# Kernel optimization log

Measured on AMD Instinct MI355X. Metric: run time of the kernel, lower is better.

The kernel has to match this reference:

```python
import jax, jax.numpy as jnp
import numpy as np
import math

DIM = 1024
NUM_HEADS = 16
HEAD_DIM = 64
SEQ_LEN = 2048
ATTN_SCALE = 0.12


def cosine_norm(x, eps=1e-12):
    # unit-normalize along last dim
    return x * jax.lax.rsqrt(jnp.sum(x * x, axis=-1, keepdims=True) + eps)


def rotary_tables(T, head_dim):
    dim_quarter = max(1, head_dim // 4)
    angular_freq = (1.0 / 1024.0) ** jnp.linspace(0.0, 1.0, dim_quarter, dtype=jnp.float32)
    angular_freq = jnp.concatenate([angular_freq, jnp.zeros(dim_quarter, dtype=jnp.float32)])  # [head_dim//2]
    t = jnp.arange(T, dtype=jnp.float32)
    theta = t[:, None] * angular_freq[None, :]  # [T, head_dim//2]
    return jnp.cos(theta), jnp.sin(theta)


def apply_rotary(x_BTHD, cos, sin):
    # cos/sin: [T, head_dim//2] -> broadcast [1, T, 1, head_dim//2]
    c = cos[None, :, None, :]
    s = sin[None, :, None, :]
    x1, x2 = jnp.split(x_BTHD, 2, axis=-1)
    y1 = x1 * c + x2 * s
    y2 = -x1 * s + x2 * c
    return jnp.concatenate([y1, y2], axis=-1)


def setup_inputs() -> dict:
    key = jax.random.key(0)
    ks = jax.random.split(key, 6)
    x = jax.random.normal(ks[0], (1, SEQ_LEN, DIM), dtype=jnp.float32)
    init_std = 0.02
    Wq = jax.random.normal(ks[1], (DIM, NUM_HEADS * HEAD_DIM), dtype=jnp.float32) * init_std
    Wk = jax.random.normal(ks[2], (DIM, NUM_HEADS * HEAD_DIM), dtype=jnp.float32) * init_std
    Wv = jax.random.normal(ks[3], (DIM, NUM_HEADS * HEAD_DIM), dtype=jnp.float32) * init_std
    Wo = jax.random.normal(ks[4], (NUM_HEADS * HEAD_DIM, DIM), dtype=jnp.float32) * init_std
    # Scale param: initialized as ones * (1/sqrt(dim)); use rand around that magnitude
    s_qk = jax.random.uniform(ks[5], (NUM_HEADS, HEAD_DIM), dtype=jnp.float32,
                              minval=0.5, maxval=1.5) * (1.0 / math.sqrt(DIM))
    return {"x": x, "Wq": Wq, "Wk": Wk, "Wv": Wv, "Wo": Wo, "s_qk": s_qk}


def reference(x, Wq, Wk, Wv, Wo, s_qk):
    B, T, _ = x.shape
    # projections
    q = (x @ Wq).reshape(B, T, NUM_HEADS, HEAD_DIM)
    k = (x @ Wk).reshape(B, T, NUM_HEADS, HEAD_DIM)
    v = (x @ Wv).reshape(B, T, NUM_HEADS, HEAD_DIM)
    # effective scale: s * (init/scale) with init=1, scale=1/sqrt(dim)
    s_eff = s_qk * math.sqrt(DIM)  # [H, D]
    q = cosine_norm(q) * s_eff[None, None, :, :]
    k = cosine_norm(k) * s_eff[None, None, :, :]
    cos, sin = rotary_tables(T, HEAD_DIM)
    q = apply_rotary(q, cos, sin)
    k = apply_rotary(k, cos, sin)
    # causal attention with fixed scale 0.12 (block_mask == causal)
    scores = jnp.einsum('bthd,bshd->bhts', q, k) * ATTN_SCALE  # [B,H,T,T]
    causal = jnp.tril(jnp.ones((T, T), dtype=bool))
    scores = jnp.where(causal[None, None, :, :], scores, jnp.float32(-1e30))
    attn = jax.nn.softmax(scores, axis=-1)
    y = jnp.einsum('bhts,bshd->bthd', attn, v)
    y = y.reshape(B, T, NUM_HEADS * HEAD_DIM)
    return y @ Wo
```

## Files before the change

kernel.cpp:

```cpp
#include <hip/hip_runtime.h>

typedef unsigned short u16;
typedef unsigned int u32;
typedef __attribute__((ext_vector_type(8))) short bf16x8;
typedef __attribute__((ext_vector_type(4))) float f32x4;

__device__ __forceinline__ u16 f2bf(float x) {
  unsigned u = __float_as_uint(x);
  u += 0x7fffu + ((u >> 16) & 1u);
  return (u16)(u >> 16);
}
__device__ __forceinline__ float bf2f(u16 z) {
  return __uint_as_float((u32)z << 16);
}

__global__ __launch_bounds__(256) void cast_kernel(const float* __restrict__ in,
                                                   u16* __restrict__ out, int n,
                                                   float2* __restrict__ rtab) {
  int g = blockIdx.x * 256 + threadIdx.x;
  int i = g * 4;
  if (i < n) {
    float4 f = *(const float4*)(in + i);
    ushort4 o;
    o.x = f2bf(f.x); o.y = f2bf(f.y); o.z = f2bf(f.z); o.w = f2bf(f.w);
    *(ushort4*)(out + i) = o;
  }
  if (g < 2048 * 16) {
    int t = g >> 4, ii = g & 15;
    float fr = exp2f(-10.0f * (float)ii / 15.0f);
    float th = (float)t * fr;
    rtab[g] = make_float2(cosf(th), sinf(th));
  }
}

__global__ __launch_bounds__(256) void transcast(const float* __restrict__ W0,
                                                 const float* __restrict__ W1,
                                                 const float* __restrict__ W2,
                                                 const float* __restrict__ W3,
                                                 u16* __restrict__ out) {
  __shared__ alignas(16) u16 ls[64 * 72];
  int z = blockIdx.z;
  const float* W = (z == 0) ? W0 : (z == 1) ? W1 : (z == 2) ? W2 : W3;
  u16* o = out + (size_t)z * (1024u * 1024u);
  int kt = blockIdx.y * 64, nt = blockIdx.x * 64;
  int tid = threadIdx.x;
  int r = tid >> 2, c0 = (tid & 3) * 16;
  const float* src = W + (size_t)(kt + r) * 1024 + nt + c0;
  u16 tmp[16];
#pragma unroll
  for (int c = 0; c < 16; c += 4) {
    float4 f = *(const float4*)(src + c);
    tmp[c + 0] = f2bf(f.x); tmp[c + 1] = f2bf(f.y);
    tmp[c + 2] = f2bf(f.z); tmp[c + 3] = f2bf(f.w);
  }
#pragma unroll
  for (int c = 0; c < 16; ++c) ls[r * 72 + c0 + c] = tmp[c];
  __syncthreads();
#pragma unroll
  for (int pass = 0; pass < 4; ++pass) {
    int n = pass * 16 + (tid >> 4);
    int kk = (tid & 15) * 4;
    ushort4 val;
    val.x = ls[(kk + 0) * 72 + n];
    val.y = ls[(kk + 1) * 72 + n];
    val.z = ls[(kk + 2) * 72 + n];
    val.w = ls[(kk + 3) * 72 + n];
    *(ushort4*)(o + (size_t)(nt + n) * 1024 + kt + kk) = val;
  }
}

#define GLD 40

__global__ __launch_bounds__(256) void gemm_qkv(const u16* __restrict__ A,
                                                const u16* __restrict__ Wt,
                                                u16* __restrict__ qb,
                                                u16* __restrict__ kb,
                                                u16* __restrict__ vt,
                                                const float* __restrict__ s_qk,
                                                const float2* __restrict__ rtab) {
  __shared__ alignas(16) u16 As[128 * GLD];
  __shared__ alignas(16) u16 Bs[128 * GLD];
  int z = blockIdx.z;
  const u16* B = Wt + (size_t)z * (1024u * 1024u);
  int tid = threadIdx.x;
  int bm = blockIdx.y * 128, bn = blockIdx.x * 128;
  int lane = tid & 63, w = tid >> 6;
  int wm = (w >> 1) * 64, wn = (w & 1) * 64;
  int m16 = lane & 15, q = lane >> 4;
  f32x4 acc[4][4] = {};
  int srow = tid >> 1, scol = (tid & 1) * 16;
  const u16* aptr = A + (size_t)(bm + srow) * 1024 + scol;
  const u16* bptr = B + (size_t)(bn + srow) * 1024 + scol;
  for (int k0 = 0; k0 < 1024; k0 += 32) {
    uint4 a0 = *(const uint4*)(aptr + k0);
    uint4 a1 = *(const uint4*)(aptr + k0 + 8);
    uint4 b0 = *(const uint4*)(bptr + k0);
    uint4 b1 = *(const uint4*)(bptr + k0 + 8);
    __syncthreads();
    *(uint4*)&As[srow * GLD + scol] = a0;
    *(uint4*)&As[srow * GLD + scol + 8] = a1;
    *(uint4*)&Bs[srow * GLD + scol] = b0;
    *(uint4*)&Bs[srow * GLD + scol + 8] = b1;
    __syncthreads();
    bf16x8 af[4], bfr[4];
#pragma unroll
    for (int mt = 0; mt < 4; ++mt)
      af[mt] = *(const bf16x8*)&As[(wm + mt * 16 + m16) * GLD + q * 8];
#pragma unroll
    for (int nt = 0; nt < 4; ++nt)
      bfr[nt] = *(const bf16x8*)&Bs[(wn + nt * 16 + m16) * GLD + q * 8];
#pragma unroll
    for (int mt = 0; mt < 4; ++mt)
#pragma unroll
      for (int nt = 0; nt < 4; ++nt)
        acc[mt][nt] = __builtin_amdgcn_mfma_f32_16x16x32_bf16(af[mt], bfr[nt], acc[mt][nt], 0, 0, 0);
  }
  int hh = (bn + wn) >> 6;
  if (z == 2) {
#pragma unroll
    for (int nt = 0; nt < 4; ++nt) {
      int n = bn + wn + nt * 16 + m16;
#pragma unroll
      for (int mt = 0; mt < 4; ++mt) {
        int t0 = bm + wm + mt * 16 + q * 4;
        ushort4 val;
        val.x = f2bf(acc[mt][nt][0]);
        val.y = f2bf(acc[mt][nt][1]);
        val.z = f2bf(acc[mt][nt][2]);
        val.w = f2bf(acc[mt][nt][3]);
        *(ushort4*)(vt + (size_t)n * 2048 + t0) = val;
      }
    }
  } else {
    u16* dst = z ? kb : qb;
    float se0 = s_qk[hh * 64 +  0 + m16] * 32.0f;
    float se1 = s_qk[hh * 64 + 16 + m16] * 32.0f;
    float se2 = s_qk[hh * 64 + 32 + m16] * 32.0f;
    float se3 = s_qk[hh * 64 + 48 + m16] * 32.0f;
#pragma unroll
    for (int mt = 0; mt < 4; ++mt)
#pragma unroll
      for (int r = 0; r < 4; ++r) {
        float ss = acc[mt][0][r] * acc[mt][0][r] + acc[mt][1][r] * acc[mt][1][r]
                 + acc[mt][2][r] * acc[mt][2][r] + acc[mt][3][r] * acc[mt][3][r];
        ss += __shfl_xor(ss, 1); ss += __shfl_xor(ss, 2);
        ss += __shfl_xor(ss, 4); ss += __shfl_xor(ss, 8);
        float inv = rsqrtf(ss + 1e-12f);
        int t = bm + wm + mt * 16 + q * 4 + r;
        float2 cs = rtab[t * 16 + m16];
        float x0 = acc[mt][0][r] * inv * se0;
        float x1 = acc[mt][1][r] * inv * se1;
        float x2 = acc[mt][2][r] * inv * se2;
        float x3 = acc[mt][3][r] * inv * se3;
        size_t off = (size_t)t * 1024 + hh * 64 + m16;
        dst[off]      = f2bf(x0 * cs.x + x2 * cs.y);
        dst[off + 16] = f2bf(x1);
        dst[off + 32] = f2bf(x2 * cs.x - x0 * cs.y);
        dst[off + 48] = f2bf(x3);
      }
  }
}

#define KH 512
__global__ __launch_bounds__(256) void gemm128(const u16* __restrict__ A,
                                               const u16* __restrict__ Bmat,
                                               float* __restrict__ C,
                                               int K, int N, size_t bz, size_t cz) {
  __shared__ alignas(16) u16 As[128 * GLD];
  __shared__ alignas(16) u16 Bs[128 * GLD];
  int z = blockIdx.z;
  const u16* B = Bmat + (size_t)(z >> 1) * bz;
  float* Cz = C + (size_t)z * cz;
  int kbeg = (z & 1) * KH;
  int tid = threadIdx.x;
  int bm = blockIdx.y * 128, bn = blockIdx.x * 128;
  int lane = tid & 63, w = tid >> 6;
  int wm = (w >> 1) * 64, wn = (w & 1) * 64;
  int m16 = lane & 15, q = lane >> 4;
  f32x4 acc[4][4] = {};
  int srow = tid >> 1, scol = (tid & 1) * 16;
  const u16* aptr = A + (size_t)(bm + srow) * K + scol;
  const u16* bptr = B + (size_t)(bn + srow) * K + scol;
  for (int k0 = kbeg; k0 < kbeg + KH; k0 += 32) {
    uint4 a0 = *(const uint4*)(aptr + k0);
    uint4 a1 = *(const uint4*)(aptr + k0 + 8);
    uint4 b0 = *(const uint4*)(bptr + k0);
    uint4 b1 = *(const uint4*)(bptr + k0 + 8);
    __syncthreads();
    *(uint4*)&As[srow * GLD + scol] = a0;
    *(uint4*)&As[srow * GLD + scol + 8] = a1;
    *(uint4*)&Bs[srow * GLD + scol] = b0;
    *(uint4*)&Bs[srow * GLD + scol + 8] = b1;
    __syncthreads();
    bf16x8 af[4], bfr[4];
#pragma unroll
    for (int mt = 0; mt < 4; ++mt)
      af[mt] = *(const bf16x8*)&As[(wm + mt * 16 + m16) * GLD + q * 8];
#pragma unroll
    for (int nt = 0; nt < 4; ++nt)
      bfr[nt] = *(const bf16x8*)&Bs[(wn + nt * 16 + m16) * GLD + q * 8];
#pragma unroll
    for (int mt = 0; mt < 4; ++mt)
#pragma unroll
      for (int nt = 0; nt < 4; ++nt)
        acc[mt][nt] = __builtin_amdgcn_mfma_f32_16x16x32_bf16(af[mt], bfr[nt], acc[mt][nt], 0, 0, 0);
  }
#pragma unroll
  for (int mt = 0; mt < 4; ++mt)
#pragma unroll
    for (int nt = 0; nt < 4; ++nt)
#pragma unroll
      for (int r = 0; r < 4; ++r) {
        int row = bm + wm + mt * 16 + q * 4 + r;
        int col = bn + wn + nt * 16 + m16;
        Cz[(size_t)row * N + col] = acc[mt][nt][r];
      }
}

__global__ __launch_bounds__(256) void addout(const float* __restrict__ p0,
                                              const float* __restrict__ p1,
                                              float* __restrict__ out, int n) {
  int i = (blockIdx.x * 256 + threadIdx.x) * 4;
  if (i >= n) return;
  float4 a = *(const float4*)(p0 + i);
  float4 b = *(const float4*)(p1 + i);
  float4 o = {a.x + b.x, a.y + b.y, a.z + b.z, a.w + b.w};
  *(float4*)(out + i) = o;
}

#define ALD 72
__global__ __launch_bounds__(256) void attn_mfma(const u16* __restrict__ qb,
                                                 const u16* __restrict__ kb,
                                                 const u16* __restrict__ vt,
                                                 u16* __restrict__ Zp,
                                                 float* __restrict__ Lp) {
  __shared__ alignas(16) u16 Ks[64 * ALD];
  __shared__ alignas(16) u16 Vt[64 * ALD];
  __shared__ alignas(16) u16 Ps[4 * 16 * ALD];
  int h = blockIdx.x;
  int qt = 31 - blockIdx.y;
  int c = blockIdx.z;
  int w4 = (qt + 4) >> 2;
  int jb = c * w4;
  int je = min(jb + w4, qt + 1);
  int slot = (h * 32 + qt) * 4 + c;
  int t0 = qt * 64;
  int tid = threadIdx.x;
  int lane = tid & 63, w = tid >> 6;
  int m16 = lane & 15, q = lane >> 4;
  u16* zout = Zp + (size_t)slot * 4096;
  float* lout = Lp + (size_t)slot * 64;
  if (jb >= je) {
#pragma unroll
    for (int nt = 0; nt < 4; ++nt)
#pragma unroll
      for (int r = 0; r < 4; ++r)
        zout[(w * 16 + q * 4 + r) * 64 + nt * 16 + m16] = 0;
    if (m16 == 0)
#pragma unroll
      for (int r = 0; r < 4; ++r) lout[w * 16 + q * 4 + r] = 0.f;
    return;
  }
  const u16* qrow = qb + (size_t)(t0 + w * 16 + m16) * 1024 + h * 64;
  bf16x8 qa0 = *(const bf16x8*)(qrow + q * 8);
  bf16x8 qa1 = *(const bf16x8*)(qrow + 32 + q * 8);
  f32x4 Yacc[4] = {};
  float lsum[4] = {0.f, 0.f, 0.f, 0.f};
  int trow = t0 + w * 16 + q * 4;
  int krow_s = tid >> 2, kcol_s = (tid & 3) * 16;
  int vd_s = tid >> 2, vk_s = (tid & 3) * 16;
  u16* pw = &Ps[w * 16 * ALD];
  for (int jt = jb; jt < je; ++jt) {
    int j0 = jt * 64;
    const u16* ksrc = kb + (size_t)(j0 + krow_s) * 1024 + h * 64 + kcol_s;
    uint4 kv0 = *(const uint4*)ksrc;
    uint4 kv1 = *(const uint4*)(ksrc + 8);
    const u16* vsrc = vt + (size_t)(h * 64 + vd_s) * 2048 + j0 + vk_s;
    uint4 vv0 = *(const uint4*)vsrc;
    uint4 vv1 = *(const uint4*)(vsrc + 8);
    __syncthreads();
    *(uint4*)&Ks[krow_s * ALD + kcol_s] = kv0;
    *(uint4*)&Ks[krow_s * ALD + kcol_s + 8] = kv1;
    *(uint4*)&Vt[vd_s * ALD + vk_s] = vv0;
    *(uint4*)&Vt[vd_s * ALD + vk_s + 8] = vv1;
    __syncthreads();
    f32x4 S[4] = {};
#pragma unroll
    for (int nt = 0; nt < 4; ++nt) {
      bf16x8 b0 = *(const bf16x8*)&Ks[(nt * 16 + m16) * ALD + q * 8];
      bf16x8 b1 = *(const bf16x8*)&Ks[(nt * 16 + m16) * ALD + 32 + q * 8];
      S[nt] = __builtin_amdgcn_mfma_f32_16x16x32_bf16(qa0, b0, S[nt], 0, 0, 0);
      S[nt] = __builtin_amdgcn_mfma_f32_16x16x32_bf16(qa1, b1, S[nt], 0, 0, 0);
    }
    bool diag = (jt == qt);
    float tmp[4] = {0.f, 0.f, 0.f, 0.f};
#pragma unroll
    for (int nt = 0; nt < 4; ++nt) {
      int j = j0 + nt * 16 + m16;
#pragma unroll
      for (int r = 0; r < 4; ++r) {
        float p = __expf(S[nt][r] * 0.12f);
        if (diag && (j > trow + r)) p = 0.f;
        tmp[r] += p;
        pw[(q * 4 + r) * ALD + nt * 16 + m16] = f2bf(p);
      }
    }
#pragma unroll
    for (int r = 0; r < 4; ++r) {
      float s = tmp[r];
      s += __shfl_xor(s, 1); s += __shfl_xor(s, 2);
      s += __shfl_xor(s, 4); s += __shfl_xor(s, 8);
      lsum[r] += s;
    }
    bf16x8 pa0 = *(const bf16x8*)&pw[m16 * ALD + q * 8];
    bf16x8 pa1 = *(const bf16x8*)&pw[m16 * ALD + 32 + q * 8];
#pragma unroll
    for (int nt = 0; nt < 4; ++nt) {
      bf16x8 b0 = *(const bf16x8*)&Vt[(nt * 16 + m16) * ALD + q * 8];
      bf16x8 b1 = *(const bf16x8*)&Vt[(nt * 16 + m16) * ALD + 32 + q * 8];
      Yacc[nt] = __builtin_amdgcn_mfma_f32_16x16x32_bf16(pa0, b0, Yacc[nt], 0, 0, 0);
      Yacc[nt] = __builtin_amdgcn_mfma_f32_16x16x32_bf16(pa1, b1, Yacc[nt], 0, 0, 0);
    }
  }
#pragma unroll
  for (int r = 0; r < 4; ++r) {
    float inv = __builtin_amdgcn_rcpf(lsum[r]);
#pragma unroll
    for (int nt = 0; nt < 4; ++nt)
      zout[(w * 16 + q * 4 + r) * 64 + nt * 16 + m16] = f2bf(Yacc[nt][r] * inv);
  }
  if (m16 == 0)
#pragma unroll
    for (int r = 0; r < 4; ++r) lout[w * 16 + q * 4 + r] = lsum[r];
}

__global__ __launch_bounds__(256) void combine(const u16* __restrict__ Zp,
                                               const float* __restrict__ Lp,
                                               u16* __restrict__ yb) {
  int tid = threadIdx.x;
  int g = blockIdx.x * 4 + (tid >> 6);
  int d = tid & 63;
  int h = g >> 11, t = g & 2047;
  int qt = t >> 6, r = t & 63;
  int base = (h * 32 + qt) * 4;
  float acc = 0.f, lt = 0.f;
#pragma unroll
  for (int c = 0; c < 4; ++c) {
    float L = Lp[(size_t)(base + c) * 64 + r];
    float z = bf2f(Zp[(size_t)(base + c) * 4096 + r * 64 + d]);
    acc += z * L;
    lt += L;
  }
  yb[(size_t)t * 1024 + h * 64 + d] = f2bf(acc / lt);
}

extern "C" void kernel_launch(void* const* d_in, const int* in_sizes, int n_in,
                              void* d_out, int out_size, void* d_ws, size_t ws_size,
                              hipStream_t stream) {
  const float* x   = (const float*)d_in[0];
  const float* Wq  = (const float*)d_in[1];
  const float* Wk  = (const float*)d_in[2];
  const float* Wv  = (const float*)d_in[3];
  const float* Wo  = (const float*)d_in[4];
  const float* sqk = (const float*)d_in[5];
  float* out = (float*)d_out;
  char* ws = (char*)d_ws;

  u16*    xb   = (u16*)ws;
  u16*    Wt   = (u16*)(ws + ((size_t)4 << 20));
  float2* rtab = (float2*)(ws + ((size_t)12 << 20));
  u16*    qb16 = (u16*)(ws + ((size_t)16 << 20));
  u16*    kb16 = (u16*)(ws + ((size_t)20 << 20));
  u16*    vt16 = (u16*)(ws + ((size_t)24 << 20));
  u16*    Zp   = (u16*)(ws + ((size_t)28 << 20));
  float*  Lp   = (float*)(ws + ((size_t)44 << 20));
  u16*    yb   = (u16*)(ws + ((size_t)45 << 20));
  float*  op   = (float*)(ws + ((size_t)49 << 20));
  u16*    Wto  = Wt + (size_t)3 * 1024 * 1024;
  const size_t PSTRIDE = (size_t)2048 * 1024;

  cast_kernel<<<2048, 256, 0, stream>>>(x, xb, 2048 * 1024, rtab);
  transcast<<<dim3(16, 16, 4), 256, 0, stream>>>(Wq, Wk, Wv, Wo, Wt);
  gemm_qkv<<<dim3(8, 16, 3), 256, 0, stream>>>(xb, Wt, qb16, kb16, vt16, sqk, rtab);
  attn_mfma<<<dim3(16, 32, 4), 256, 0, stream>>>(qb16, kb16, vt16, Zp, Lp);
  combine<<<8192, 256, 0, stream>>>(Zp, Lp, yb);
  gemm128<<<dim3(8, 16, 2), 256, 0, stream>>>(yb, Wto, op, 1024, 1024, 0, PSTRIDE);
  addout<<<2048, 256, 0, stream>>>(op, op + PSTRIDE, out, 2048 * 1024);
}
```

Measured before the change: 164.0 us.

## Fold causal attention tiles, drop split-K combine, and prefetch GEMM loads

```diff
diff --git a/kernel.cpp b/kernel.cpp
--- a/kernel.cpp
+++ b/kernel.cpp
@@ -91,16 +91,23 @@
   int srow = tid >> 1, scol = (tid & 1) * 16;
   const u16* aptr = A + (size_t)(bm + srow) * 1024 + scol;
   const u16* bptr = B + (size_t)(bn + srow) * 1024 + scol;
+  uint4 a0 = *(const uint4*)(aptr);
+  uint4 a1 = *(const uint4*)(aptr + 8);
+  uint4 b0 = *(const uint4*)(bptr);
+  uint4 b1 = *(const uint4*)(bptr + 8);
   for (int k0 = 0; k0 < 1024; k0 += 32) {
-    uint4 a0 = *(const uint4*)(aptr + k0);
-    uint4 a1 = *(const uint4*)(aptr + k0 + 8);
-    uint4 b0 = *(const uint4*)(bptr + k0);
-    uint4 b1 = *(const uint4*)(bptr + k0 + 8);
     __syncthreads();
     *(uint4*)&As[srow * GLD + scol] = a0;
     *(uint4*)&As[srow * GLD + scol + 8] = a1;
     *(uint4*)&Bs[srow * GLD + scol] = b0;
     *(uint4*)&Bs[srow * GLD + scol + 8] = b1;
+    uint4 na0, na1, nb0, nb1;
+    if (k0 < 992) {
+      na0 = *(const uint4*)(aptr + k0 + 32);
+      na1 = *(const uint4*)(aptr + k0 + 40);
+      nb0 = *(const uint4*)(bptr + k0 + 32);
+      nb1 = *(const uint4*)(bptr + k0 + 40);
+    }
     __syncthreads();
     bf16x8 af[4], bfr[4];
 #pragma unroll
@@ -114,6 +121,7 @@
 #pragma unroll
       for (int nt = 0; nt < 4; ++nt)
         acc[mt][nt] = __builtin_amdgcn_mfma_f32_16x16x32_bf16(af[mt], bfr[nt], acc[mt][nt], 0, 0, 0);
+    if (k0 < 992) { a0 = na0; a1 = na1; b0 = nb0; b1 = nb1; }
   }
   int hh = (bn + wn) >> 6;
   if (z == 2) {
@@ -161,197 +169,158 @@
   }
 }
 
-#define KH 512
-__global__ __launch_bounds__(256) void gemm128(const u16* __restrict__ A,
-                                               const u16* __restrict__ Bmat,
-                                               float* __restrict__ C,
-                                               int K, int N, size_t bz, size_t cz) {
-  __shared__ alignas(16) u16 As[128 * GLD];
-  __shared__ alignas(16) u16 Bs[128 * GLD];
-  int z = blockIdx.z;
-  const u16* B = Bmat + (size_t)(z >> 1) * bz;
-  float* Cz = C + (size_t)z * cz;
-  int kbeg = (z & 1) * KH;
-  int tid = threadIdx.x;
-  int bm = blockIdx.y * 128, bn = blockIdx.x * 128;
-  int lane = tid & 63, w = tid >> 6;
-  int wm = (w >> 1) * 64, wn = (w & 1) * 64;
-  int m16 = lane & 15, q = lane >> 4;
-  f32x4 acc[4][4] = {};
-  int srow = tid >> 1, scol = (tid & 1) * 16;
-  const u16* aptr = A + (size_t)(bm + srow) * K + scol;
-  const u16* bptr = B + (size_t)(bn + srow) * K + scol;
-  for (int k0 = kbeg; k0 < kbeg + KH; k0 += 32) {
-    uint4 a0 = *(const uint4*)(aptr + k0);
-    uint4 a1 = *(const uint4*)(aptr + k0 + 8);
-    uint4 b0 = *(const uint4*)(bptr + k0);
-    uint4 b1 = *(const uint4*)(bptr + k0 + 8);
-    __syncthreads();
-    *(uint4*)&As[srow * GLD + scol] = a0;
-    *(uint4*)&As[srow * GLD + scol + 8] = a1;
-    *(uint4*)&Bs[srow * GLD + scol] = b0;
-    *(uint4*)&Bs[srow * GLD + scol + 8] = b1;
-    __syncthreads();
-    bf16x8 af[4], bfr[4];
-#pragma unroll
-    for (int mt = 0; mt < 4; ++mt)
-      af[mt] = *(const bf16x8*)&As[(wm + mt * 16 + m16) * GLD + q * 8];
-#pragma unroll
-    for (int nt = 0; nt < 4; ++nt)
-      bfr[nt] = *(const bf16x8*)&Bs[(wn + nt * 16 + m16) * GLD + q * 8];
-#pragma unroll
-    for (int mt = 0; mt < 4; ++mt)
-#pragma unroll
-      for (int nt = 0; nt < 4; ++nt)
-        acc[mt][nt] = __builtin_amdgcn_mfma_f32_16x16x32_bf16(af[mt], bfr[nt], acc[mt][nt], 0, 0, 0);
-  }
-#pragma unroll
-  for (int mt = 0; mt < 4; ++mt)
-#pragma unroll
-    for (int nt = 0; nt < 4; ++nt)
-#pragma unroll
-      for (int r = 0; r < 4; ++r) {
-        int row = bm + wm + mt * 16 + q * 4 + r;
-        int col = bn + wn + nt * 16 + m16;
-        Cz[(size_t)row * N + col] = acc[mt][nt][r];
-      }
-}
-
-__global__ __launch_bounds__(256) void addout(const float* __restrict__ p0,
-                                              const float* __restrict__ p1,
-                                              float* __restrict__ out, int n) {
-  int i = (blockIdx.x * 256 + threadIdx.x) * 4;
-  if (i >= n) return;
-  float4 a = *(const float4*)(p0 + i);
-  float4 b = *(const float4*)(p1 + i);
-  float4 o = {a.x + b.x, a.y + b.y, a.z + b.z, a.w + b.w};
-  *(float4*)(out + i) = o;
-}
-
 #define ALD 72
-__global__ __launch_bounds__(256) void attn_mfma(const u16* __restrict__ qb,
+__global__ __launch_bounds__(256) void attn_fold(const u16* __restrict__ qb,
                                                  const u16* __restrict__ kb,
                                                  const u16* __restrict__ vt,
-                                                 u16* __restrict__ Zp,
-                                                 float* __restrict__ Lp) {
+                                                 u16* __restrict__ yb) {
   __shared__ alignas(16) u16 Ks[64 * ALD];
   __shared__ alignas(16) u16 Vt[64 * ALD];
   __shared__ alignas(16) u16 Ps[4 * 16 * ALD];
   int h = blockIdx.x;
-  int qt = 31 - blockIdx.y;
-  int c = blockIdx.z;
-  int w4 = (qt + 4) >> 2;
-  int jb = c * w4;
-  int je = min(jb + w4, qt + 1);
-  int slot = (h * 32 + qt) * 4 + c;
-  int t0 = qt * 64;
+  int y = blockIdx.y;
   int tid = threadIdx.x;
   int lane = tid & 63, w = tid >> 6;
   int m16 = lane & 15, q = lane >> 4;
-  u16* zout = Zp + (size_t)slot * 4096;
-  float* lout = Lp + (size_t)slot * 64;
-  if (jb >= je) {
+  int krow_s = tid >> 2, kcol_s = (tid & 3) * 16;
+  const u16* kbase = kb + (size_t)krow_s * 1024 + h * 64 + kcol_s;
+  const u16* vbase = vt + (size_t)(h * 64 + krow_s) * 2048 + kcol_s;
+  u16* pw = &Ps[w * 16 * ALD];
+#pragma unroll 1
+  for (int half = 0; half < 2; ++half) {
+    int qt = half ? y : 31 - y;
+    int t0 = qt * 64;
+    const u16* qrow = qb + (size_t)(t0 + w * 16 + m16) * 1024 + h * 64;
+    bf16x8 qa0 = *(const bf16x8*)(qrow + q * 8);
+    bf16x8 qa1 = *(const bf16x8*)(qrow + 32 + q * 8);
+    f32x4 Yacc[4] = {};
+    float lsum[4] = {0.f, 0.f, 0.f, 0.f};
+    int trow = t0 + w * 16 + q * 4;
+    uint4 kv0 = *(const uint4*)kbase;
+    uint4 kv1 = *(const uint4*)(kbase + 8);
+    uint4 vv0 = *(const uint4*)vbase;
+    uint4 vv1 = *(const uint4*)(vbase + 8);
+    for (int jt = 0; jt <= qt; ++jt) {
+      __syncthreads();
+      *(uint4*)&Ks[krow_s * ALD + kcol_s] = kv0;
+      *(uint4*)&Ks[krow_s * ALD + kcol_s + 8] = kv1;
+      *(uint4*)&Vt[krow_s * ALD + kcol_s] = vv0;
+      *(uint4*)&Vt[krow_s * ALD + kcol_s + 8] = vv1;
+      uint4 kn0, kn1, vn0, vn1;
+      if (jt < qt) {
+        const u16* kp = kbase + (size_t)(jt + 1) * 65536;
+        const u16* vp = vbase + (jt + 1) * 64;
+        kn0 = *(const uint4*)kp;
+        kn1 = *(const uint4*)(kp + 8);
+        vn0 = *(const uint4*)vp;
+        vn1 = *(const uint4*)(vp + 8);
+      }
+      __syncthreads();
+      f32x4 S[4] = {};
+#pragma unroll
+      for (int nt = 0; nt < 4; ++nt) {
+        bf16x8 b0 = *(const bf16x8*)&Ks[(nt * 16 + m16) * ALD + q * 8];
+        bf16x8 b1 = *(const bf16x8*)&Ks[(nt * 16 + m16) * ALD + 32 + q * 8];
+        S[nt] = __builtin_amdgcn_mfma_f32_16x16x32_bf16(qa0, b0, S[nt], 0, 0, 0);
+        S[nt] = __builtin_amdgcn_mfma_f32_16x16x32_bf16(qa1, b1, S[nt], 0, 0, 0);
+      }
+      bool diag = (jt == qt);
+      int j0 = jt * 64;
+      float tmp[4] = {0.f, 0.f, 0.f, 0.f};
+#pragma unroll
+      for (int nt = 0; nt < 4; ++nt) {
+        int j = j0 + nt * 16 + m16;
+#pragma unroll
+        for (int r = 0; r < 4; ++r) {
+          float p = __builtin_amdgcn_exp2f(S[nt][r] * 0.17312340490667562f);
+          if (diag && (j > trow + r)) p = 0.f;
+          tmp[r] += p;
+          pw[(q * 4 + r) * ALD + nt * 16 + m16] = f2bf(p);
+        }
+      }
+#pragma unroll
+      for (int r = 0; r < 4; ++r) {
+        float s = tmp[r];
+        s += __shfl_xor(s, 1); s += __shfl_xor(s, 2);
+        s += __shfl_xor(s, 4); s += __shfl_xor(s, 8);
+        lsum[r] += s;
+      }
+      bf16x8 pa0 = *(const bf16x8*)&pw[m16 * ALD + q * 8];
+      bf16x8 pa1 = *(const bf16x8*)&pw[m16 * ALD + 32 + q * 8];
+#pragma unroll
+      for (int nt = 0; nt < 4; ++nt) {
+        bf16x8 b0 = *(const bf16x8*)&Vt[(nt * 16 + m16) * ALD + q * 8];
+        bf16x8 b1 = *(const bf16x8*)&Vt[(nt * 16 + m16) * ALD + 32 + q * 8];
+        Yacc[nt] = __builtin_amdgcn_mfma_f32_16x16x32_bf16(pa0, b0, Yacc[nt], 0, 0, 0);
+        Yacc[nt] = __builtin_amdgcn_mfma_f32_16x16x32_bf16(pa1, b1, Yacc[nt], 0, 0, 0);
+      }
+      if (jt < qt) { kv0 = kn0; kv1 = kn1; vv0 = vn0; vv1 = vn1; }
+    }
+#pragma unroll
+    for (int r = 0; r < 4; ++r) {
+      float inv = __builtin_amdgcn_rcpf(lsum[r]);
+      int t = t0 + w * 16 + q * 4 + r;
+#pragma unroll
+      for (int nt = 0; nt < 4; ++nt)
+        yb[(size_t)t * 1024 + h * 64 + nt * 16 + m16] = f2bf(Yacc[nt][r] * inv);
+    }
+  }
+}
+
+__global__ __launch_bounds__(256) void gemm_o(const u16* __restrict__ A,
+                                              const u16* __restrict__ B,
+                                              float* __restrict__ C) {
+  __shared__ alignas(16) u16 As[128 * GLD];
+  __shared__ alignas(16) u16 Bs[64 * GLD];
+  int tid = threadIdx.x;
+  int bm = blockIdx.y * 128, bn = blockIdx.x * 64;
+  int lane = tid & 63, w = tid >> 6;
+  int wm = w * 32;
+  int m16 = lane & 15, q = lane >> 4;
+  f32x4 acc[2][4] = {};
+  int srA = tid >> 1, scA = (tid & 1) * 16;
+  int srB = tid >> 2, scB = (tid & 3) * 8;
+  const u16* aptr = A + (size_t)(bm + srA) * 1024 + scA;
+  const u16* bptr = B + (size_t)(bn + srB) * 1024 + scB;
+  uint4 a0 = *(const uint4*)(aptr);
+  uint4 a1 = *(const uint4*)(aptr + 8);
+  uint4 b0 = *(const uint4*)(bptr);
+  for (int k0 = 0; k0 < 1024; k0 += 32) {
+    __syncthreads();
+    *(uint4*)&As[srA * GLD + scA] = a0;
+    *(uint4*)&As[srA * GLD + scA + 8] = a1;
+    *(uint4*)&Bs[srB * GLD + scB] = b0;
+    uint4 na0, na1, nb0;
+    if (k0 < 992) {
+      na0 = *(const uint4*)(aptr + k0 + 32);
+      na1 = *(const uint4*)(aptr + k0 + 40);
+      nb0 = *(const uint4*)(bptr + k0 + 32);
+    }
+    __syncthreads();
+    bf16x8 af[2], bfr[4];
+#pragma unroll
+    for (int mt = 0; mt < 2; ++mt)
+      af[mt] = *(const bf16x8*)&As[(wm + mt * 16 + m16) * GLD + q * 8];
 #pragma unroll
     for (int nt = 0; nt < 4; ++nt)
-#pragma unroll
-      for (int r = 0; r < 4; ++r)
-        zout[(w * 16 + q * 4 + r) * 64 + nt * 16 + m16] = 0;
-    if (m16 == 0)
-#pragma unroll
-      for (int r = 0; r < 4; ++r) lout[w * 16 + q * 4 + r] = 0.f;
-    return;
-  }
-  const u16* qrow = qb + (size_t)(t0 + w * 16 + m16) * 1024 + h * 64;
-  bf16x8 qa0 = *(const bf16x8*)(qrow + q * 8);
-  bf16x8 qa1 = *(const bf16x8*)(qrow + 32 + q * 8);
-  f32x4 Yacc[4] = {};
-  float lsum[4] = {0.f, 0.f, 0.f, 0.f};
-  int trow = t0 + w * 16 + q * 4;
-  int krow_s = tid >> 2, kcol_s = (tid & 3) * 16;
-  int vd_s = tid >> 2, vk_s = (tid & 3) * 16;
-  u16* pw = &Ps[w * 16 * ALD];
-  for (int jt = jb; jt < je; ++jt) {
-    int j0 = jt * 64;
-    const u16* ksrc = kb + (size_t)(j0 + krow_s) * 1024 + h * 64 + kcol_s;
-    uint4 kv0 = *(const uint4*)ksrc;
-    uint4 kv1 = *(const uint4*)(ksrc + 8);
-    const u16* vsrc = vt + (size_t)(h * 64 + vd_s) * 2048 + j0 + vk_s;
-    uint4 vv0 = *(const uint4*)vsrc;
-    uint4 vv1 = *(const uint4*)(vsrc + 8);
-    __syncthreads();
-    *(uint4*)&Ks[krow_s * ALD + kcol_s] = kv0;
-    *(uint4*)&Ks[krow_s * ALD + kcol_s + 8] = kv1;
-    *(uint4*)&Vt[vd_s * ALD + vk_s] = vv0;
-    *(uint4*)&Vt[vd_s * ALD + vk_s + 8] = vv1;
-    __syncthreads();
-    f32x4 S[4] = {};
-#pragma unroll
-    for (int nt = 0; nt < 4; ++nt) {
-      bf16x8 b0 = *(const bf16x8*)&Ks[(nt * 16 + m16) * ALD + q * 8];
-      bf16x8 b1 = *(const bf16x8*)&Ks[(nt * 16 + m16) * ALD + 32 + q * 8];
-      S[nt] = __builtin_amdgcn_mfma_f32_16x16x32_bf16(qa0, b0, S[nt], 0, 0, 0);
-      S[nt] = __builtin_amdgcn_mfma_f32_16x16x32_bf16(qa1, b1, S[nt], 0, 0, 0);
-    }
-    bool diag = (jt == qt);
-    float tmp[4] = {0.f, 0.f, 0.f, 0.f};
-#pragma unroll
-    for (int nt = 0; nt < 4; ++nt) {
-      int j = j0 + nt * 16 + m16;
+      bfr[nt] = *(const bf16x8*)&Bs[(nt * 16 + m16) * GLD + q * 8];
+#pragma unroll
+    for (int mt = 0; mt < 2; ++mt)
+#pragma unroll
+      for (int nt = 0; nt < 4; ++nt)
+        acc[mt][nt] = __builtin_amdgcn_mfma_f32_16x16x32_bf16(af[mt], bfr[nt], acc[mt][nt], 0, 0, 0);
+    if (k0 < 992) { a0 = na0; a1 = na1; b0 = nb0; }
+  }
+#pragma unroll
+  for (int mt = 0; mt < 2; ++mt)
+#pragma unroll
+    for (int nt = 0; nt < 4; ++nt)
 #pragma unroll
       for (int r = 0; r < 4; ++r) {
-        float p = __expf(S[nt][r] * 0.12f);
-        if (diag && (j > trow + r)) p = 0.f;
-        tmp[r] += p;
-        pw[(q * 4 + r) * ALD + nt * 16 + m16] = f2bf(p);
-      }
-    }
-#pragma unroll
-    for (int r = 0; r < 4; ++r) {
-      float s = tmp[r];
-      s += __shfl_xor(s, 1); s += __shfl_xor(s, 2);
-      s += __shfl_xor(s, 4); s += __shfl_xor(s, 8);
-      lsum[r] += s;
-    }
-    bf16x8 pa0 = *(const bf16x8*)&pw[m16 * ALD + q * 8];
-    bf16x8 pa1 = *(const bf16x8*)&pw[m16 * ALD + 32 + q * 8];
-#pragma unroll
-    for (int nt = 0; nt < 4; ++nt) {
-      bf16x8 b0 = *(const bf16x8*)&Vt[(nt * 16 + m16) * ALD + q * 8];
-      bf16x8 b1 = *(const bf16x8*)&Vt[(nt * 16 + m16) * ALD + 32 + q * 8];
-      Yacc[nt] = __builtin_amdgcn_mfma_f32_16x16x32_bf16(pa0, b0, Yacc[nt], 0, 0, 0);
-      Yacc[nt] = __builtin_amdgcn_mfma_f32_16x16x32_bf16(pa1, b1, Yacc[nt], 0, 0, 0);
-    }
-  }
-#pragma unroll
-  for (int r = 0; r < 4; ++r) {
-    float inv = __builtin_amdgcn_rcpf(lsum[r]);
-#pragma unroll
-    for (int nt = 0; nt < 4; ++nt)
-      zout[(w * 16 + q * 4 + r) * 64 + nt * 16 + m16] = f2bf(Yacc[nt][r] * inv);
-  }
-  if (m16 == 0)
-#pragma unroll
-    for (int r = 0; r < 4; ++r) lout[w * 16 + q * 4 + r] = lsum[r];
-}
-
-__global__ __launch_bounds__(256) void combine(const u16* __restrict__ Zp,
-                                               const float* __restrict__ Lp,
-                                               u16* __restrict__ yb) {
-  int tid = threadIdx.x;
-  int g = blockIdx.x * 4 + (tid >> 6);
-  int d = tid & 63;
-  int h = g >> 11, t = g & 2047;
-  int qt = t >> 6, r = t & 63;
-  int base = (h * 32 + qt) * 4;
-  float acc = 0.f, lt = 0.f;
-#pragma unroll
-  for (int c = 0; c < 4; ++c) {
-    float L = Lp[(size_t)(base + c) * 64 + r];
-    float z = bf2f(Zp[(size_t)(base + c) * 4096 + r * 64 + d]);
-    acc += z * L;
-    lt += L;
-  }
-  yb[(size_t)t * 1024 + h * 64 + d] = f2bf(acc / lt);
+        int row = bm + wm + mt * 16 + q * 4 + r;
+        int col = bn + nt * 16 + m16;
+        C[(size_t)row * 1024 + col] = acc[mt][nt][r];
+      }
 }
 
 extern "C" void kernel_launch(void* const* d_in, const int* in_sizes, int n_in,
@@ -372,18 +341,12 @@
   u16*    qb16 = (u16*)(ws + ((size_t)16 << 20));
   u16*    kb16 = (u16*)(ws + ((size_t)20 << 20));
   u16*    vt16 = (u16*)(ws + ((size_t)24 << 20));
-  u16*    Zp   = (u16*)(ws + ((size_t)28 << 20));
-  float*  Lp   = (float*)(ws + ((size_t)44 << 20));
-  u16*    yb   = (u16*)(ws + ((size_t)45 << 20));
-  float*  op   = (float*)(ws + ((size_t)49 << 20));
+  u16*    yb   = (u16*)(ws + ((size_t)28 << 20));
   u16*    Wto  = Wt + (size_t)3 * 1024 * 1024;
-  const size_t PSTRIDE = (size_t)2048 * 1024;
 
   cast_kernel<<<2048, 256, 0, stream>>>(x, xb, 2048 * 1024, rtab);
   transcast<<<dim3(16, 16, 4), 256, 0, stream>>>(Wq, Wk, Wv, Wo, Wt);
   gemm_qkv<<<dim3(8, 16, 3), 256, 0, stream>>>(xb, Wt, qb16, kb16, vt16, sqk, rtab);
-  attn_mfma<<<dim3(16, 32, 4), 256, 0, stream>>>(qb16, kb16, vt16, Zp, Lp);
-  combine<<<8192, 256, 0, stream>>>(Zp, Lp, yb);
-  gemm128<<<dim3(8, 16, 2), 256, 0, stream>>>(yb, Wto, op, 1024, 1024, 0, PSTRIDE);
-  addout<<<2048, 256, 0, stream>>>(op, op + PSTRIDE, out, 2048 * 1024);
-}
+  attn_fold<<<dim3(16, 16), 256, 0, stream>>>(qb16, kb16, vt16, yb);
+  gemm_o<<<dim3(16, 16), 256, 0, stream>>>(yb, Wto, out);
+}
```

After: 153.5 us. 6.4% less time.
